# Performance work log

Measured on AMD Instinct MI355X. Metric: run time of the kernel, lower is better.

The kernel has to match this reference:

```python
import jax, jax.numpy as jnp
import numpy as np

D_MODEL = 1024
N_HEADS = 16
D_K = 64
D_FF = 4 * D_MODEL
LN_EPS = 1e-5


def _ln(x, g, b):
    mu = jnp.mean(x, axis=-1, keepdims=True)
    var = jnp.mean((x - mu) ** 2, axis=-1, keepdims=True)
    return (x - mu) * jax.lax.rsqrt(var + LN_EPS) * g + b


def setup_inputs() -> dict:
    key = jax.random.key(0)
    ks = jax.random.split(key, 24)
    d, h, dk, dff = D_MODEL, N_HEADS, D_K, D_FF
    s = lambda k, sh, fan: jax.random.normal(k, sh, jnp.float32) / np.sqrt(fan)
    return {
        "x": jax.random.normal(ks[0], (2, 2048, d), jnp.float32),
        "mask": jnp.ones((2, 2048), jnp.int32),
        # pre-attention q/k/v embed linears (d -> d)
        "Wqe": s(ks[1], (d, d), d), "bqe": jnp.zeros((d,), jnp.float32),
        "Wke": s(ks[2], (d, d), d), "bke": jnp.zeros((d,), jnp.float32),
        "Wve": s(ks[3], (d, d), d), "bve": jnp.zeros((d,), jnp.float32),
        # MHA projections (d -> h*dk) and output fc
        "Wq": s(ks[4], (d, h * dk), d), "bq": jnp.zeros((h * dk,), jnp.float32),
        "Wk": s(ks[5], (d, h * dk), d), "bk": jnp.zeros((h * dk,), jnp.float32),
        "Wv": s(ks[6], (d, h * dk), d), "bv": jnp.zeros((h * dk,), jnp.float32),
        "Wo": s(ks[7], (h * dk, d), h * dk), "bo": jnp.zeros((d,), jnp.float32),
        # layer norms
        "g1": jnp.ones((d,), jnp.float32), "b1": jnp.zeros((d,), jnp.float32),
        "g2": jnp.ones((d,), jnp.float32), "b2": jnp.zeros((d,), jnp.float32),
        # FFN
        "W1": s(ks[8], (d, dff), d), "bb1": jnp.zeros((dff,), jnp.float32),
        "W2": s(ks[9], (dff, d), dff), "bb2": jnp.zeros((d,), jnp.float32),
    }


def reference(x, mask, Wqe, bqe, Wke, bke, Wve, bve, Wq, bq, Wk, bk, Wv, bv,
              Wo, bo, g1, b1, g2, b2, W1, bb1, W2, bb2):
    N, T, _ = x.shape
    h, dk = N_HEADS, D_K
    # pre-embeds then MHA projections
    q = ((x @ Wqe + bqe) @ Wq + bq).reshape(N, T, h, dk)
    k = ((x @ Wke + bke) @ Wk + bk).reshape(N, T, h, dk)
    v = ((x @ Wve + bve) @ Wv + bv).reshape(N, T, h, dk)
    scores = jnp.einsum("bthd,bshd->bhts", q, k) / np.sqrt(dk).astype(np.float32)
    scores = jnp.where(mask[:, None, None, :] == 0, -jnp.inf, scores)
    attn = jax.nn.softmax(scores, axis=-1)
    a = jnp.einsum("bhts,bshd->bthd", attn, v).reshape(N, T, h * dk)
    mha_out = a @ Wo + bo
    x = _ln(x + mha_out, g1, b1)
    ffn = jax.nn.gelu(x @ W1 + bb1, approximate=False) @ W2 + bb2
    x = _ln(x + ffn, g2, b2)
    return x  # dropout is identity in eval mode
```

## Files before the change

### kernel.cpp

```cpp
#include <hip/hip_runtime.h>
#include <stdint.h>
#include <math.h>


#define DM   1024
#define DFF  4096
#define NH   16
#define DKH  64
#define TSEQ 2048
#define TOK  4096

using f32x4  = float  __attribute__((ext_vector_type(4)));
using bf16x8 = __bf16 __attribute__((ext_vector_type(8)));
using s16x8  = short  __attribute__((ext_vector_type(8)));

typedef const void __attribute__((address_space(1)))* gas_ptr;
typedef void       __attribute__((address_space(3)))* las_ptr;

__device__ __forceinline__ short f2bf(float f) {
  unsigned u; __builtin_memcpy(&u, &f, 4);
  u += 0x7FFFu + ((u >> 16) & 1u);
  return (short)(u >> 16);
}
__device__ __forceinline__ float bf2f(short s) {
  unsigned u = ((unsigned)(unsigned short)s) << 16;
  float f; __builtin_memcpy(&f, &u, 4);
  return f;
}
__device__ __forceinline__ unsigned cvt_pk_bf16(float lo, float hi) {
  unsigned r;
  asm volatile("v_cvt_pk_bf16_f32 %0, %1, %2" : "=v"(r) : "v"(lo), "v"(hi));
  return r;
}
__device__ __forceinline__ f32x4 mfma16(s16x8 a, s16x8 b, f32x4 c) {
  return __builtin_amdgcn_mfma_f32_16x16x32_bf16(
      __builtin_bit_cast(bf16x8, a), __builtin_bit_cast(bf16x8, b), c, 0, 0, 0);
}
__device__ __forceinline__ void gload16(const void* g, void* l) {
  __builtin_amdgcn_global_load_lds((gas_ptr)g, (las_ptr)l, 16, 0, 0);
}

__global__ void cvt_bf16(const float* __restrict__ S, short* __restrict__ D, long n) {
  long i = ((long)blockIdx.x * 256 + threadIdx.x) * 8;
  if (i >= n) return;
  float4 a = *(const float4*)(S + i);
  float4 b = *(const float4*)(S + i + 4);
  s16x8 o;
  o[0]=f2bf(a.x); o[1]=f2bf(a.y); o[2]=f2bf(a.z); o[3]=f2bf(a.w);
  o[4]=f2bf(b.x); o[5]=f2bf(b.y); o[6]=f2bf(b.z); o[7]=f2bf(b.w);
  *(s16x8*)(D + i) = o;
}

__global__ __launch_bounds__(256) void transpose_cvt(const float* __restrict__ W,
                                                     short* __restrict__ WT, int R, int C) {
  __shared__ float t[64][65];
  const int c0 = blockIdx.x * 64, r0 = blockIdx.y * 64;
  const int tr = threadIdx.x >> 4, tc = (threadIdx.x & 15) * 4;
  #pragma unroll
  for (int q = 0; q < 4; q++) {
    int rr = q * 16 + tr;
    float4 v = *(const float4*)(W + (long)(r0 + rr) * C + c0 + tc);
    t[rr][tc] = v.x; t[rr][tc+1] = v.y; t[rr][tc+2] = v.z; t[rr][tc+3] = v.w;
  }
  __syncthreads();
  #pragma unroll
  for (int q = 0; q < 4; q++) {
    int rr = q * 16 + tr;
    short4 o;
    o.x = f2bf(t[tc+0][rr]); o.y = f2bf(t[tc+1][rr]);
    o.z = f2bf(t[tc+2][rr]); o.w = f2bf(t[tc+3][rr]);
    *(short4*)(WT + (long)(c0 + rr) * R + r0 + tc) = o;
  }
}

struct BiasArgs {
  const float* be[3]; const short* WT[3]; const float* b2[3]; float* bc[3]; int K;
};
__global__ void fuse_bias(BiasArgs a) {
  const int z = blockIdx.y, n = blockIdx.x, lane = threadIdx.x;
  const float* be = a.be[z];
  const short* WT = a.WT[z] + (long)n * a.K;
  float s = 0.f;
  for (int k = lane; k < a.K; k += 64) s += be[k] * bf2f(WT[k]);
  #pragma unroll
  for (int d = 1; d < 64; d <<= 1) s += __shfl_xor(s, d);
  if (lane == 0) a.bc[z][n] = s + a.b2[z][n];
}

struct GemmArgs {
  const short* A[3]; const short* B[3]; const float* bias[3]; void* C[3];
  float oscale[3];
  int M, N, K;
  int tmask;
};

template<int EPI>
__global__ __launch_bounds__(256) void gemm_bt(GemmArgs g) {
  const int z = blockIdx.z;
  const short* __restrict__ A = g.A[z];
  const short* __restrict__ B = g.B[z];
  const float* __restrict__ bias = g.bias[z];
  const int N = g.N, K = g.K;
  const int tn = blockIdx.x * 128, tm = blockIdx.y * 128;
  const int lane = threadIdx.x & 63, w = threadIdx.x >> 6;
  const int wr = w >> 1, wc = w & 1;

  __shared__ alignas(16) short lA[128 * 64];
  __shared__ alignas(16) short lB[128 * 64];

  f32x4 acc[4][4] = {};

  const int srow = lane >> 3;
  const int scol = lane & 7;

  for (int k0 = 0; k0 < K; k0 += 64) {
    #pragma unroll
    for (int q = 0; q < 4; q++) {
      const int row  = w * 32 + q * 8 + srow;
      const int slot = scol ^ (row & 7);
      gload16(A + (long)(tm + row) * K + k0 + slot * 8, lA + (w * 32 + q * 8) * 64);
      gload16(B + (long)(tn + row) * K + k0 + slot * 8, lB + (w * 32 + q * 8) * 64);
    }
    __syncthreads();
    #pragma unroll
    for (int kk = 0; kk < 2; kk++) {
      s16x8 af[4], bfr[4];
      #pragma unroll
      for (int m = 0; m < 4; m++) {
        const int row = wr * 64 + m * 16 + (lane & 15);
        const int ps  = (kk * 4 + (lane >> 4)) ^ (row & 7);
        af[m] = *(const s16x8*)(lA + row * 64 + ps * 8);
      }
      #pragma unroll
      for (int n = 0; n < 4; n++) {
        const int row = wc * 64 + n * 16 + (lane & 15);
        const int ps  = (kk * 4 + (lane >> 4)) ^ (row & 7);
        bfr[n] = *(const s16x8*)(lB + row * 64 + ps * 8);
      }
      #pragma unroll
      for (int m = 0; m < 4; m++)
        #pragma unroll
        for (int n = 0; n < 4; n++)
          acc[m][n] = mfma16(af[m], bfr[n], acc[m][n]);
    }
    __syncthreads();
  }

  const bool outT = (g.tmask >> z) & 1;
  const float sc = g.oscale[z];
  #pragma unroll
  for (int n = 0; n < 4; n++) {
    const int col = tn + wc * 64 + n * 16 + (lane & 15);
    const float bv = bias ? bias[col] : 0.f;
    #pragma unroll
    for (int m = 0; m < 4; m++) {
      const int row0 = tm + wr * 64 + m * 16 + (lane >> 4) * 4;
      float v[4];
      #pragma unroll
      for (int r = 0; r < 4; r++) {
        float x = (acc[m][n][r] + bv) * sc;
        if (EPI == 2) x = 0.5f * x * (1.f + erff(x * 0.70710678f));
        v[r] = x;
      }
      if (EPI == 1) {
        float* C = (float*)g.C[z];
        #pragma unroll
        for (int r = 0; r < 4; r++) C[(long)(row0 + r) * N + col] = v[r];
      } else if (!outT) {
        short* C = (short*)g.C[z];
        #pragma unroll
        for (int r = 0; r < 4; r++) C[(long)(row0 + r) * N + col] = f2bf(v[r]);
      } else {
        short* C = (short*)g.C[z];
        short4 o;
        o.x = f2bf(v[0]); o.y = f2bf(v[1]); o.z = f2bf(v[2]); o.w = f2bf(v[3]);
        *(short4*)(C + (long)col * g.M + row0) = o;
      }
    }
  }
}

__global__ __launch_bounds__(256) void flash_attn(const short* __restrict__ Q,
                                                  const short* __restrict__ Km,
                                                  const short* __restrict__ VT,
                                                  const int* __restrict__ mask,
                                                  short* __restrict__ O) {
  const int qt = blockIdx.x;
  const int bh = blockIdx.y;
  const int b = bh >> 4, h = bh & 15;
  const int lane = threadIdx.x & 63, w = threadIdx.x >> 6;
  const int g2 = lane >> 4, q = lane & 15;

  __shared__ alignas(16) short lK[2][64 * 64];
  __shared__ alignas(16) short lV[2][64 * 64];
  __shared__ alignas(16) short lP[4][16 * 64];

  const int qrow0 = b * TSEQ + qt * 64 + w * 16;

  s16x8 qf[2];
  #pragma unroll
  for (int kk = 0; kk < 2; kk++)
    qf[kk] = *(const s16x8*)(Q + (long)(qrow0 + q) * DM + h * DKH + kk * 32 + g2 * 8);

  float lI = 0.f;
  f32x4 oacc[4] = {};

  const int srow = lane >> 3, scol = lane & 7;
  short* lPw = &lP[w][0];
  const int psw = (q & 7) << 3;

  const int nt = TSEQ / 64;
  #pragma unroll
  for (int t2 = 0; t2 < 2; t2++) {
    const int row  = w * 16 + t2 * 8 + srow;
    const int slot = scol ^ (row & 7);
    gload16(Km + (long)(b * TSEQ + row) * DM + h * DKH + slot * 8,
            &lK[0][(w * 16 + t2 * 8) * 64]);
    gload16(VT + (long)(h * DKH + row) * TOK + b * TSEQ + slot * 8,
            &lV[0][(w * 16 + t2 * 8) * 64]);
  }

  for (int t = 0; t < nt; t++) {
    const int cb = t & 1;
    const short* lKc = &lK[cb][0];
    const short* lVc = &lV[cb][0];
    __syncthreads();

    if (t + 1 < nt) {
      const int kvn = (t + 1) * 64;
      #pragma unroll
      for (int t2 = 0; t2 < 2; t2++) {
        const int row  = w * 16 + t2 * 8 + srow;
        const int slot = scol ^ (row & 7);
        gload16(Km + (long)(b * TSEQ + kvn + row) * DM + h * DKH + slot * 8,
                &lK[cb ^ 1][(w * 16 + t2 * 8) * 64]);
        gload16(VT + (long)(h * DKH + row) * TOK + b * TSEQ + kvn + slot * 8,
                &lV[cb ^ 1][(w * 16 + t2 * 8) * 64]);
      }
    }
    const int mk = mask[b * TSEQ + t * 64 + lane];

    f32x4 s[4] = {};
    __builtin_amdgcn_s_setprio(1);
    #pragma unroll
    for (int kk = 0; kk < 2; kk++)
      #pragma unroll
      for (int n = 0; n < 4; n++) {
        const int row = n * 16 + q;
        const int ps  = (kk * 4 + g2) ^ (row & 7);
        s16x8 kf = *(const s16x8*)(lKc + row * 64 + ps * 8);
        s[n] = mfma16(kf, qf[kk], s[n]);
      }
    __builtin_amdgcn_s_setprio(0);

    float p[4][4];
    #pragma unroll
    for (int n = 0; n < 4; n++)
      #pragma unroll
      for (int r = 0; r < 4; r++)
        p[n][r] = exp2f(s[n][r]);

    if (__ballot(mk == 0)) {
      const float mzf = mk ? 1.f : 0.f;
      #pragma unroll
      for (int n = 0; n < 4; n++)
        #pragma unroll
        for (int r = 0; r < 4; r++)
          p[n][r] *= __shfl(mzf, n * 16 + g2 * 4 + r);
    }
    #pragma unroll
    for (int n = 0; n < 4; n++)
      lI += (p[n][0] + p[n][1]) + (p[n][2] + p[n][3]);

    #pragma unroll
    for (int n = 0; n < 4; n++)
      #pragma unroll
      for (int hh = 0; hh < 2; hh++) {
        unsigned pk = cvt_pk_bf16(p[n][2 * hh], p[n][2 * hh + 1]);
        *(unsigned*)(lPw + ((q * 64 + n * 16 + g2 * 4 + 2 * hh) ^ psw)) = pk;
      }
    s16x8 pf[2];
    #pragma unroll
    for (int kk = 0; kk < 2; kk++)
      pf[kk] = *(const s16x8*)(lPw + ((q * 64 + kk * 32 + g2 * 8) ^ psw));

    __builtin_amdgcn_s_setprio(1);
    #pragma unroll
    for (int kk = 0; kk < 2; kk++)
      #pragma unroll
      for (int n = 0; n < 4; n++) {
        const int row = n * 16 + q;
        const int ps  = (kk * 4 + g2) ^ (row & 7);
        s16x8 vf = *(const s16x8*)(lVc + row * 64 + ps * 8);
        oacc[n] = mfma16(pf[kk], vf, oacc[n]);
      }
    __builtin_amdgcn_s_setprio(0);
  }

  lI += __shfl_xor(lI, 16);
  lI += __shfl_xor(lI, 32);
  float rI[4];
  #pragma unroll
  for (int r = 0; r < 4; r++) rI[r] = 1.f / __shfl(lI, g2 * 4 + r);
  #pragma unroll
  for (int n = 0; n < 4; n++) {
    const int col = h * DKH + n * 16 + q;
    #pragma unroll
    for (int r = 0; r < 4; r++) {
      const int row = qrow0 + g2 * 4 + r;
      O[(long)row * DM + col] = f2bf(oacc[n][r] * rI[r]);
    }
  }
}

template<bool WB16>
__global__ __launch_bounds__(256) void ln_residual(const float* __restrict__ X,
                                                   const float* __restrict__ R,
                                                   const float* __restrict__ gw,
                                                   const float* __restrict__ bw,
                                                   float* __restrict__ Yf,
                                                   short* __restrict__ Yb) {
  const int row = blockIdx.x, tid = threadIdx.x;
  const float4 xv = *(const float4*)(X + (long)row * DM + tid * 4);
  const float4 rv = *(const float4*)(R + (long)row * DM + tid * 4);
  float v[4] = {xv.x + rv.x, xv.y + rv.y, xv.z + rv.z, xv.w + rv.w};
  float s  = v[0] + v[1] + v[2] + v[3];
  float s2 = v[0]*v[0] + v[1]*v[1] + v[2]*v[2] + v[3]*v[3];
  #pragma unroll
  for (int d = 1; d < 64; d <<= 1) { s += __shfl_xor(s, d); s2 += __shfl_xor(s2, d); }
  __shared__ float red[8];
  const int lane = tid & 63, w = tid >> 6;
  if (lane == 0) { red[w] = s; red[w + 4] = s2; }
  __syncthreads();
  s  = red[0] + red[1] + red[2] + red[3];
  s2 = red[4] + red[5] + red[6] + red[7];
  const float mu  = s * (1.f / DM);
  const float inv = rsqrtf(s2 * (1.f / DM) - mu * mu + 1e-5f);
  #pragma unroll
  for (int i = 0; i < 4; i++) {
    const int col = tid * 4 + i;
    const float y = (v[i] - mu) * inv * gw[col] + bw[col];
    Yf[(long)row * DM + col] = y;
    if (WB16) Yb[(long)row * DM + col] = f2bf(y);
  }
}

extern "C" void kernel_launch(void* const* d_in, const int* in_sizes, int n_in,
                              void* d_out, int out_size, void* d_ws, size_t ws_size,
                              hipStream_t stream) {
  const float* x   = (const float*)d_in[0];
  const int*   msk = (const int*)d_in[1];
  const float* Wqe = (const float*)d_in[2];  const float* bqe = (const float*)d_in[3];
  const float* Wke = (const float*)d_in[4];  const float* bke = (const float*)d_in[5];
  const float* Wve = (const float*)d_in[6];  const float* bve = (const float*)d_in[7];
  const float* Wq  = (const float*)d_in[8];  const float* bq  = (const float*)d_in[9];
  const float* Wk  = (const float*)d_in[10]; const float* bk  = (const float*)d_in[11];
  const float* Wv  = (const float*)d_in[12]; const float* bv  = (const float*)d_in[13];
  const float* Wo  = (const float*)d_in[14]; const float* bo  = (const float*)d_in[15];
  const float* g1  = (const float*)d_in[16]; const float* b1  = (const float*)d_in[17];
  const float* g2  = (const float*)d_in[18]; const float* b2  = (const float*)d_in[19];
  const float* W1  = (const float*)d_in[20]; const float* bb1 = (const float*)d_in[21];
  const float* W2  = (const float*)d_in[22]; const float* bb2 = (const float*)d_in[23];

  char* ws = (char*)d_ws;
  const size_t MB = 1024ull * 1024ull;
  short* xb   = (short*)(ws + 0);
  short* woT  = (short*)(ws + 8 * MB);
  short* w1T  = (short*)(ws + 10 * MB);
  short* w2T  = (short*)(ws + 18 * MB);
  short* wqeB = (short*)(ws + 26 * MB);
  short* wkeB = (short*)(ws + 28 * MB);
  short* wveB = (short*)(ws + 30 * MB);
  short* wqT  = (short*)(ws + 32 * MB);
  short* wkT  = (short*)(ws + 34 * MB);
  short* wvT  = (short*)(ws + 36 * MB);
  short* wcqT = (short*)(ws + 38 * MB);
  short* wckT = (short*)(ws + 40 * MB);
  short* wcvT = (short*)(ws + 42 * MB);
  float* bcq  = (float*)(ws + 44 * MB);
  float* bck  = (float*)(ws + 44 * MB + 16384);
  float* bcv  = (float*)(ws + 44 * MB + 32768);
  short* Qb   = (short*)(ws + 45 * MB);
  short* Kb2  = (short*)(ws + 53 * MB);
  short* VTb  = (short*)(ws + 61 * MB);
  short* Hb   = (short*)(ws + 26 * MB);
  float* yf   = (float*)(ws + 58 * MB);
  short* ybf  = (short*)(ws + 74 * MB);
  short* Aout = xb;
  float* mha  = (float*)d_out;
  float* Ff   = (float*)d_out;

  cvt_bf16<<<dim3((long)TOK * DM / 2048), 256, 0, stream>>>(x, xb, (long)TOK * DM);
  cvt_bf16<<<dim3((long)DM * DM / 2048), 256, 0, stream>>>(Wqe, wqeB, (long)DM * DM);
  cvt_bf16<<<dim3((long)DM * DM / 2048), 256, 0, stream>>>(Wke, wkeB, (long)DM * DM);
  cvt_bf16<<<dim3((long)DM * DM / 2048), 256, 0, stream>>>(Wve, wveB, (long)DM * DM);
  transpose_cvt<<<dim3(16, 16), 256, 0, stream>>>(Wq, wqT, DM, DM);
  transpose_cvt<<<dim3(16, 16), 256, 0, stream>>>(Wk, wkT, DM, DM);
  transpose_cvt<<<dim3(16, 16), 256, 0, stream>>>(Wv, wvT, DM, DM);
  transpose_cvt<<<dim3(16, 16), 256, 0, stream>>>(Wo, woT, DM, DM);
  transpose_cvt<<<dim3(64, 16), 256, 0, stream>>>(W1, w1T, DM, DFF);
  transpose_cvt<<<dim3(16, 64), 256, 0, stream>>>(W2, w2T, DFF, DM);

  GemmArgs fa = {};
  fa.A[0] = wqT;  fa.A[1] = wkT;  fa.A[2] = wvT;
  fa.B[0] = wqeB; fa.B[1] = wkeB; fa.B[2] = wveB;
  fa.C[0] = wcqT; fa.C[1] = wckT; fa.C[2] = wcvT;
  fa.oscale[0] = 1.f; fa.oscale[1] = 1.f; fa.oscale[2] = 1.f;
  fa.M = DM; fa.N = DM; fa.K = DM; fa.tmask = 0;
  gemm_bt<0><<<dim3(8, 8, 3), 256, 0, stream>>>(fa);

  BiasArgs ba = {};
  ba.be[0] = bqe; ba.be[1] = bke; ba.be[2] = bve;
  ba.WT[0] = wqT; ba.WT[1] = wkT; ba.WT[2] = wvT;
  ba.b2[0] = bq;  ba.b2[1] = bk;  ba.b2[2] = bv;
  ba.bc[0] = bcq; ba.bc[1] = bck; ba.bc[2] = bcv; ba.K = DM;
  fuse_bias<<<dim3(DM, 3), 64, 0, stream>>>(ba);

  GemmArgs qa = {};
  qa.A[0] = xb;   qa.A[1] = xb;   qa.A[2] = xb;
  qa.B[0] = wcqT; qa.B[1] = wckT; qa.B[2] = wcvT;
  qa.bias[0] = bcq; qa.bias[1] = bck; qa.bias[2] = bcv;
  qa.C[0] = Qb; qa.C[1] = Kb2; qa.C[2] = VTb;
  qa.oscale[0] = 0.125f * 1.44269504f; qa.oscale[1] = 1.f; qa.oscale[2] = 1.f;
  qa.M = TOK; qa.N = DM; qa.K = DM; qa.tmask = 4;
  gemm_bt<0><<<dim3(8, 32, 3), 256, 0, stream>>>(qa);

  flash_attn<<<dim3(TSEQ / 64, 2 * NH), 256, 0, stream>>>(Qb, Kb2, VTb, msk, Aout);

  GemmArgs oa = {};
  oa.A[0] = Aout; oa.B[0] = woT; oa.bias[0] = bo; oa.C[0] = mha;
  oa.oscale[0] = 1.f;
  oa.M = TOK; oa.N = DM; oa.K = DM; oa.tmask = 0;
  gemm_bt<1><<<dim3(8, 32, 1), 256, 0, stream>>>(oa);

  ln_residual<true><<<dim3(TOK), 256, 0, stream>>>(x, mha, g1, b1, yf, ybf);

  GemmArgs f1 = {};
  f1.A[0] = ybf; f1.B[0] = w1T; f1.bias[0] = bb1; f1.C[0] = Hb;
  f1.oscale[0] = 1.f;
  f1.M = TOK; f1.N = DFF; f1.K = DM; f1.tmask = 0;
  gemm_bt<2><<<dim3(32, 32, 1), 256, 0, stream>>>(f1);

  GemmArgs f2 = {};
  f2.A[0] = Hb; f2.B[0] = w2T; f2.bias[0] = bb2; f2.C[0] = Ff;
  f2.oscale[0] = 1.f;
  f2.M = TOK; f2.N = DM; f2.K = DFF; f2.tmask = 0;
  gemm_bt<1><<<dim3(8, 32, 1), 256, 0, stream>>>(f2);

  ln_residual<false><<<dim3(TOK), 256, 0, stream>>>(yf, Ff, g2, b2, (float*)d_out, nullptr);
}
```

Baseline: 345.8 us.

## Split-K the N=1024 output GEMMs and sum partials in layernorm; batch conversion launches

The Wo projection and the second FFN GEMM, which have only 256 tiles each, are now split along K into two slices. Each slice writes an fp32 partial, and the residual layernorm kernel adds both partials plus the bias. This doubles the block count to fill more compute units. The cost is extra fp32 partial traffic and one more read in the layernorm. The several cvt_bf16 and transpose_cvt launches are also merged into batched launches to cut launch overhead.

```diff
diff --git a/kernel.cpp b/kernel.cpp
--- a/kernel.cpp
+++ b/kernel.cpp
@@ -40,20 +40,27 @@
   __builtin_amdgcn_global_load_lds((gas_ptr)g, (las_ptr)l, 16, 0, 0);
 }
 
-__global__ void cvt_bf16(const float* __restrict__ S, short* __restrict__ D, long n) {
+struct CvtArgs { const float* S[4]; short* D[4]; long n[4]; };
+__global__ void cvt_bf16_b(CvtArgs a) {
+  const int z = blockIdx.y;
   long i = ((long)blockIdx.x * 256 + threadIdx.x) * 8;
-  if (i >= n) return;
-  float4 a = *(const float4*)(S + i);
-  float4 b = *(const float4*)(S + i + 4);
+  if (i >= a.n[z]) return;
+  const float* S = a.S[z]; short* D = a.D[z];
+  float4 va = *(const float4*)(S + i);
+  float4 vb = *(const float4*)(S + i + 4);
   s16x8 o;
-  o[0]=f2bf(a.x); o[1]=f2bf(a.y); o[2]=f2bf(a.z); o[3]=f2bf(a.w);
-  o[4]=f2bf(b.x); o[5]=f2bf(b.y); o[6]=f2bf(b.z); o[7]=f2bf(b.w);
+  o[0]=f2bf(va.x); o[1]=f2bf(va.y); o[2]=f2bf(va.z); o[3]=f2bf(va.w);
+  o[4]=f2bf(vb.x); o[5]=f2bf(vb.y); o[6]=f2bf(vb.z); o[7]=f2bf(vb.w);
   *(s16x8*)(D + i) = o;
 }
 
-__global__ __launch_bounds__(256) void transpose_cvt(const float* __restrict__ W,
-                                                     short* __restrict__ WT, int R, int C) {
+struct TcvtArgs { const float* W[4]; short* WT[4]; };
+template<int NZ>
+__global__ __launch_bounds__(256) void transpose_cvt(TcvtArgs a, int R, int C) {
   __shared__ float t[64][65];
+  const int z = (NZ > 1) ? blockIdx.z : 0;
+  const float* __restrict__ W = a.W[z];
+  short* __restrict__ WT = a.WT[z];
   const int c0 = blockIdx.x * 64, r0 = blockIdx.y * 64;
   const int tr = threadIdx.x >> 4, tc = (threadIdx.x & 15) * 4;
   #pragma unroll
@@ -88,19 +95,24 @@
 }
 
 struct GemmArgs {
-  const short* A[3]; const short* B[3]; const float* bias[3]; void* C[3];
+  const short* A[3]; const short* B[3]; const float* bias[3]; void* C[6];
   float oscale[3];
   int M, N, K;
   int tmask;
+  int zshift;
 };
 
 template<int EPI>
 __global__ __launch_bounds__(256) void gemm_bt(GemmArgs g) {
-  const int z = blockIdx.z;
-  const short* __restrict__ A = g.A[z];
-  const short* __restrict__ B = g.B[z];
-  const float* __restrict__ bias = g.bias[z];
+  const int zz = blockIdx.z;
+  const int prob = zz >> g.zshift;
+  const int slice = zz & ((1 << g.zshift) - 1);
+  const short* __restrict__ A = g.A[prob];
+  const short* __restrict__ B = g.B[prob];
+  const float* __restrict__ bias = g.bias[prob];
   const int N = g.N, K = g.K;
+  const int Ks = K >> g.zshift;
+  const int kbase = slice * Ks;
   const int tn = blockIdx.x * 128, tm = blockIdx.y * 128;
   const int lane = threadIdx.x & 63, w = threadIdx.x >> 6;
   const int wr = w >> 1, wc = w & 1;
@@ -113,13 +125,15 @@
   const int srow = lane >> 3;
   const int scol = lane & 7;
 
-  for (int k0 = 0; k0 < K; k0 += 64) {
+  for (int k0 = 0; k0 < Ks; k0 += 64) {
     #pragma unroll
     for (int q = 0; q < 4; q++) {
       const int row  = w * 32 + q * 8 + srow;
       const int slot = scol ^ (row & 7);
-      gload16(A + (long)(tm + row) * K + k0 + slot * 8, lA + (w * 32 + q * 8) * 64);
-      gload16(B + (long)(tn + row) * K + k0 + slot * 8, lB + (w * 32 + q * 8) * 64);
+      gload16(A + (long)(tm + row) * K + kbase + k0 + slot * 8,
+              lA + (w * 32 + q * 8) * 64);
+      gload16(B + (long)(tn + row) * K + kbase + k0 + slot * 8,
+              lB + (w * 32 + q * 8) * 64);
     }
     __syncthreads();
     #pragma unroll
@@ -146,8 +160,8 @@
     __syncthreads();
   }
 
-  const bool outT = (g.tmask >> z) & 1;
-  const float sc = g.oscale[z];
+  const bool outT = (g.tmask >> prob) & 1;
+  const float sc = g.oscale[prob];
   #pragma unroll
   for (int n = 0; n < 4; n++) {
     const int col = tn + wc * 64 + n * 16 + (lane & 15);
@@ -163,15 +177,15 @@
         v[r] = x;
       }
       if (EPI == 1) {
-        float* C = (float*)g.C[z];
+        float* C = (float*)g.C[zz];
         #pragma unroll
         for (int r = 0; r < 4; r++) C[(long)(row0 + r) * N + col] = v[r];
       } else if (!outT) {
-        short* C = (short*)g.C[z];
+        short* C = (short*)g.C[zz];
         #pragma unroll
         for (int r = 0; r < 4; r++) C[(long)(row0 + r) * N + col] = f2bf(v[r]);
       } else {
-        short* C = (short*)g.C[z];
+        short* C = (short*)g.C[zz];
         short4 o;
         o.x = f2bf(v[0]); o.y = f2bf(v[1]); o.z = f2bf(v[2]); o.w = f2bf(v[3]);
         *(short4*)(C + (long)col * g.M + row0) = o;
@@ -315,15 +329,20 @@
 
 template<bool WB16>
 __global__ __launch_bounds__(256) void ln_residual(const float* __restrict__ X,
-                                                   const float* __restrict__ R,
+                                                   const float* __restrict__ P0,
+                                                   const float* __restrict__ P1,
+                                                   const float* __restrict__ rbias,
                                                    const float* __restrict__ gw,
                                                    const float* __restrict__ bw,
                                                    float* __restrict__ Yf,
                                                    short* __restrict__ Yb) {
   const int row = blockIdx.x, tid = threadIdx.x;
   const float4 xv = *(const float4*)(X + (long)row * DM + tid * 4);
-  const float4 rv = *(const float4*)(R + (long)row * DM + tid * 4);
-  float v[4] = {xv.x + rv.x, xv.y + rv.y, xv.z + rv.z, xv.w + rv.w};
+  const float4 p0 = *(const float4*)(P0 + (long)row * DM + tid * 4);
+  const float4 p1 = *(const float4*)(P1 + (long)row * DM + tid * 4);
+  const float4 rb = *(const float4*)(rbias + tid * 4);
+  float v[4] = {xv.x + p0.x + p1.x + rb.x, xv.y + p0.y + p1.y + rb.y,
+                xv.z + p0.z + p1.z + rb.z, xv.w + p0.w + p1.w + rb.w};
   float s  = v[0] + v[1] + v[2] + v[3];
   float s2 = v[0]*v[0] + v[1]*v[1] + v[2]*v[2] + v[3]*v[3];
   #pragma unroll
@@ -383,30 +402,37 @@
   short* Qb   = (short*)(ws + 45 * MB);
   short* Kb2  = (short*)(ws + 53 * MB);
   short* VTb  = (short*)(ws + 61 * MB);
+  float* mhaP0= (float*)(ws + 26 * MB);
+  float* mhaP1= (float*)(ws + 42 * MB);
   short* Hb   = (short*)(ws + 26 * MB);
   float* yf   = (float*)(ws + 58 * MB);
   short* ybf  = (short*)(ws + 74 * MB);
+  float* ffnP0= (float*)d_out;
+  float* ffnP1= (float*)(ws + 0);
   short* Aout = xb;
-  float* mha  = (float*)d_out;
-  float* Ff   = (float*)d_out;
-
-  cvt_bf16<<<dim3((long)TOK * DM / 2048), 256, 0, stream>>>(x, xb, (long)TOK * DM);
-  cvt_bf16<<<dim3((long)DM * DM / 2048), 256, 0, stream>>>(Wqe, wqeB, (long)DM * DM);
-  cvt_bf16<<<dim3((long)DM * DM / 2048), 256, 0, stream>>>(Wke, wkeB, (long)DM * DM);
-  cvt_bf16<<<dim3((long)DM * DM / 2048), 256, 0, stream>>>(Wve, wveB, (long)DM * DM);
-  transpose_cvt<<<dim3(16, 16), 256, 0, stream>>>(Wq, wqT, DM, DM);
-  transpose_cvt<<<dim3(16, 16), 256, 0, stream>>>(Wk, wkT, DM, DM);
-  transpose_cvt<<<dim3(16, 16), 256, 0, stream>>>(Wv, wvT, DM, DM);
-  transpose_cvt<<<dim3(16, 16), 256, 0, stream>>>(Wo, woT, DM, DM);
-  transpose_cvt<<<dim3(64, 16), 256, 0, stream>>>(W1, w1T, DM, DFF);
-  transpose_cvt<<<dim3(16, 64), 256, 0, stream>>>(W2, w2T, DFF, DM);
+
+  CvtArgs ca = {};
+  ca.S[0] = x;  ca.D[0] = xb;   ca.n[0] = (long)TOK * DM;
+  ca.S[1] = Wqe; ca.D[1] = wqeB; ca.n[1] = (long)DM * DM;
+  ca.S[2] = Wke; ca.D[2] = wkeB; ca.n[2] = (long)DM * DM;
+  ca.S[3] = Wve; ca.D[3] = wveB; ca.n[3] = (long)DM * DM;
+  cvt_bf16_b<<<dim3((long)TOK * DM / 2048, 4), 256, 0, stream>>>(ca);
+
+  TcvtArgs t4 = {};
+  t4.W[0] = Wq; t4.WT[0] = wqT;  t4.W[1] = Wk; t4.WT[1] = wkT;
+  t4.W[2] = Wv; t4.WT[2] = wvT;  t4.W[3] = Wo; t4.WT[3] = woT;
+  transpose_cvt<4><<<dim3(16, 16, 4), 256, 0, stream>>>(t4, DM, DM);
+  TcvtArgs t1 = {}; t1.W[0] = W1; t1.WT[0] = w1T;
+  transpose_cvt<1><<<dim3(64, 16), 256, 0, stream>>>(t1, DM, DFF);
+  TcvtArgs t2 = {}; t2.W[0] = W2; t2.WT[0] = w2T;
+  transpose_cvt<1><<<dim3(16, 64), 256, 0, stream>>>(t2, DFF, DM);
 
   GemmArgs fa = {};
   fa.A[0] = wqT;  fa.A[1] = wkT;  fa.A[2] = wvT;
   fa.B[0] = wqeB; fa.B[1] = wkeB; fa.B[2] = wveB;
   fa.C[0] = wcqT; fa.C[1] = wckT; fa.C[2] = wcvT;
   fa.oscale[0] = 1.f; fa.oscale[1] = 1.f; fa.oscale[2] = 1.f;
-  fa.M = DM; fa.N = DM; fa.K = DM; fa.tmask = 0;
+  fa.M = DM; fa.N = DM; fa.K = DM; fa.tmask = 0; fa.zshift = 0;
   gemm_bt<0><<<dim3(8, 8, 3), 256, 0, stream>>>(fa);
 
   BiasArgs ba = {};
@@ -422,30 +448,34 @@
   qa.bias[0] = bcq; qa.bias[1] = bck; qa.bias[2] = bcv;
   qa.C[0] = Qb; qa.C[1] = Kb2; qa.C[2] = VTb;
   qa.oscale[0] = 0.125f * 1.44269504f; qa.oscale[1] = 1.f; qa.oscale[2] = 1.f;
-  qa.M = TOK; qa.N = DM; qa.K = DM; qa.tmask = 4;
+  qa.M = TOK; qa.N = DM; qa.K = DM; qa.tmask = 4; qa.zshift = 0;
   gemm_bt<0><<<dim3(8, 32, 3), 256, 0, stream>>>(qa);
 
   flash_attn<<<dim3(TSEQ / 64, 2 * NH), 256, 0, stream>>>(Qb, Kb2, VTb, msk, Aout);
 
   GemmArgs oa = {};
-  oa.A[0] = Aout; oa.B[0] = woT; oa.bias[0] = bo; oa.C[0] = mha;
+  oa.A[0] = Aout; oa.B[0] = woT; oa.bias[0] = nullptr;
+  oa.C[0] = mhaP0; oa.C[1] = mhaP1;
   oa.oscale[0] = 1.f;
-  oa.M = TOK; oa.N = DM; oa.K = DM; oa.tmask = 0;
-  gemm_bt<1><<<dim3(8, 32, 1), 256, 0, stream>>>(oa);
-
-  ln_residual<true><<<dim3(TOK), 256, 0, stream>>>(x, mha, g1, b1, yf, ybf);
+  oa.M = TOK; oa.N = DM; oa.K = DM; oa.tmask = 0; oa.zshift = 1;
+  gemm_bt<1><<<dim3(8, 32, 2), 256, 0, stream>>>(oa);
+
+  ln_residual<true><<<dim3(TOK), 256, 0, stream>>>(x, mhaP0, mhaP1, bo,
+                                                   g1, b1, yf, ybf);
 
   GemmArgs f1 = {};
   f1.A[0] = ybf; f1.B[0] = w1T; f1.bias[0] = bb1; f1.C[0] = Hb;
   f1.oscale[0] = 1.f;
-  f1.M = TOK; f1.N = DFF; f1.K = DM; f1.tmask = 0;
+  f1.M = TOK; f1.N = DFF; f1.K = DM; f1.tmask = 0; f1.zshift = 0;
   gemm_bt<2><<<dim3(32, 32, 1), 256, 0, stream>>>(f1);
 
   GemmArgs f2 = {};
-  f2.A[0] = Hb; f2.B[0] = w2T; f2.bias[0] = bb2; f2.C[0] = Ff;
+  f2.A[0] = Hb; f2.B[0] = w2T; f2.bias[0] = nullptr;
+  f2.C[0] = ffnP0; f2.C[1] = ffnP1;
   f2.oscale[0] = 1.f;
-  f2.M = TOK; f2.N = DM; f2.K = DFF; f2.tmask = 0;
-  gemm_bt<1><<<dim3(8, 32, 1), 256, 0, stream>>>(f2);
-
-  ln_residual<false><<<dim3(TOK), 256, 0, stream>>>(yf, Ff, g2, b2, (float*)d_out, nullptr);
-}
+  f2.M = TOK; f2.N = DM; f2.K = DFF; f2.tmask = 0; f2.zshift = 1;
+  gemm_bt<1><<<dim3(8, 32, 2), 256, 0, stream>>>(f2);
+
+  ln_residual<false><<<dim3(TOK), 256, 0, stream>>>(yf, ffnP0, ffnP1, bb2,
+                                                    g2, b2, (float*)d_out, nullptr);
+}
```

New measurement: 302.4 us. -12.5%, faster.
